# Optimization experiments

Hardware: AMD Instinct MI355X
Metric: run time of the kernel (lower is better)

## Reference

```python
import jax, jax.numpy as jnp
import numpy as np

TAU_MEM = 20.0
V_THRESH = 1.0
DECAY = float(np.exp(-1.0 / TAU_MEM))
SLOPE = 5.0  # fast-sigmoid surrogate slope


@jax.custom_vjp
def spike(x):
    # Heaviside spike with fast-sigmoid surrogate gradient
    return (x > 0).astype(x.dtype)

def _spike_fwd(x):
    return spike(x), x

def _spike_bwd(x, g):
    surr = 1.0 / (1.0 + SLOPE * jnp.abs(x)) ** 2
    return (g * surr,)

spike.defvjp(_spike_fwd, _spike_bwd)


def setup_inputs() -> dict:
    key = jax.random.key(0)
    k1, k2 = jax.random.split(key)
    B, T, n_in, n_out = 32, 1000, 1024, 512
    input_spikes_seq = (jax.random.uniform(k1, (B, T, n_in)) < 0.05).astype(jnp.float32)
    w_init_scale = 0.5
    W = jax.random.normal(k2, (n_out, n_in), dtype=jnp.float32) * (w_init_scale / np.sqrt(n_in))
    return {"input_spikes_seq": input_spikes_seq, "W": W}


def reference(input_spikes_seq, W):
    # input_spikes_seq: (B, T, n_in); W: (n_out, n_in) -> out: (B, T, n_out)
    B, T, _ = input_spikes_seq.shape
    n_out = W.shape[0]
    # Hoist the GEMM out of the time loop: (B,T,n_in) x (n_out,n_in) -> (B,T,n_out)
    I = jnp.einsum('bti,oi->bto', input_spikes_seq, W)
    I_t = jnp.transpose(I, (1, 0, 2))  # (T, B, n_out)

    def step(v, i_t):
        v = v * DECAY + i_t
        s = spike(v - V_THRESH)
        v = v * (1.0 - jax.lax.stop_gradient(s))  # reset, detached as in torch
        return v, s

    v0 = jnp.zeros((B, n_out), dtype=input_spikes_seq.dtype)
    _, out_t = jax.lax.scan(step, v0, I_t)  # out_t: (T, B, n_out)
    return jnp.transpose(out_t, (1, 0, 2))
```

## Files before the change

### kernel.cpp

```cpp
#include <hip/hip_runtime.h>


#define N_IN   1024
#define N_OUT  512
#define DECAY_F 0.95122942450071400910f
#define SCALE     17179869184.0
#define SCALE_INV 5.8207660913467407e-11f

typedef int  v4i  __attribute__((ext_vector_type(4)));
typedef int  v16i __attribute__((ext_vector_type(16)));

__global__ __launch_bounds__(256) void s_to_i8(const float* __restrict__ S,
                                               signed char* __restrict__ S8,
                                               int n16) {
    const int g = blockIdx.x * 256 + threadIdx.x;
    if (g >= n16) return;
    const float4* p = reinterpret_cast<const float4*>(S) + (size_t)g * 4;
    union { signed char c[16]; int4 v; } u;
#pragma unroll
    for (int q = 0; q < 4; ++q) {
        const float4 v = p[q];
        u.c[q * 4 + 0] = (signed char)(v.x != 0.f);
        u.c[q * 4 + 1] = (signed char)(v.y != 0.f);
        u.c[q * 4 + 2] = (signed char)(v.z != 0.f);
        u.c[q * 4 + 3] = (signed char)(v.w != 0.f);
    }
    reinterpret_cast<int4*>(S8)[g] = u.v;
}

__global__ __launch_bounds__(256) void w_digits(const float* __restrict__ W,
                                                signed char* __restrict__ D8) {
    const int n  = blockIdx.x;
    const int k0 = threadIdx.x * 4;
    const float4 wv = *reinterpret_cast<const float4*>(W + (size_t)n * N_IN + k0);
    const float ww[4] = {wv.x, wv.y, wv.z, wv.w};
    int pk[4] = {0, 0, 0, 0};
#pragma unroll
    for (int j = 0; j < 4; ++j) {
        long long wi = (long long)rint((double)ww[j] * SCALE);
        const int d0 = (int)((wi + 128) & 255) - 128; wi = (wi - d0) >> 8;
        const int d1 = (int)((wi + 128) & 255) - 128; wi = (wi - d1) >> 8;
        const int d2 = (int)((wi + 128) & 255) - 128; wi = (wi - d2) >> 8;
        const int d3 = (int)wi;
        pk[0] |= (d0 & 255) << (8 * j);
        pk[1] |= (d1 & 255) << (8 * j);
        pk[2] |= (d2 & 255) << (8 * j);
        pk[3] |= (d3 & 255) << (8 * j);
    }
#pragma unroll
    for (int d = 0; d < 4; ++d)
        *reinterpret_cast<int*>(D8 + (size_t)(d * N_OUT + n) * N_IN + k0) = pk[d];
}

#define BM 256
#define BN 64
#define BK 64
#define PITCH 80
#define ABUF (BM * PITCH)
#define ASH(buf) (lds + (buf) * ABUF)
#define BSH(buf) (lds + 2 * ABUF + (buf) * ABUF)

__global__ __launch_bounds__(512, 2) void gemm_i8(
        const signed char* __restrict__ S8,
        const signed char* __restrict__ D8,
        float* __restrict__ I, int M) {
    extern __shared__ signed char lds[];

    const int tid  = threadIdx.x;
    const int lane = tid & 63;
    const int w    = tid >> 6;
    const int wwm  = w >> 1;
    const int wwn  = w & 1;

    const int nx  = M / BM;
    const int u   = (blockIdx.x & 7) * nx + (blockIdx.x >> 3);
    const int bm  = u >> 3;
    const int bn  = u & 7;
    const int m0 = bm * BM;
    const int n0 = bn * BN;

    const int srow = tid >> 2;
    const int scol = (tid & 3) * 16;

    v16i acc[2][4];
#pragma unroll
    for (int mf = 0; mf < 2; ++mf)
#pragma unroll
        for (int d = 0; d < 4; ++d)
#pragma unroll
            for (int i = 0; i < 16; ++i) acc[mf][d][i] = 0;

    int4 pa0, pa1, pb0, pb1;
    int4 qa0, qa1, qb0, qb1;

#define LOADT(SET, kt)                                                            \
    SET##a0 = *reinterpret_cast<const int4*>(S8 + (size_t)(m0 + srow) * N_IN + (kt) * BK + scol);        \
    SET##a1 = *reinterpret_cast<const int4*>(S8 + (size_t)(m0 + srow + 128) * N_IN + (kt) * BK + scol);  \
    SET##b0 = *reinterpret_cast<const int4*>(D8 + (size_t)(((srow >> 6) * N_OUT) + n0 + (srow & 63)) * N_IN + (kt) * BK + scol);            \
    SET##b1 = *reinterpret_cast<const int4*>(D8 + (size_t)(((srow >> 6) * N_OUT + 2 * N_OUT) + n0 + (srow & 63)) * N_IN + (kt) * BK + scol);

#define WRITET(buf, SET)                                                          \
    *reinterpret_cast<int4*>(ASH(buf) + (srow) * PITCH + scol) = SET##a0;         \
    *reinterpret_cast<int4*>(ASH(buf) + (srow + 128) * PITCH + scol) = SET##a1;   \
    *reinterpret_cast<int4*>(BSH(buf) + (srow) * PITCH + scol) = SET##b0;         \
    *reinterpret_cast<int4*>(BSH(buf) + (srow + 128) * PITCH + scol) = SET##b1;

    const int fr = lane & 31;
    const int kh = (lane >> 5) * 16;

#define COMPUTE(buf)                                                              \
    _Pragma("unroll")                                                             \
    for (int ksub = 0; ksub < 2; ++ksub) {                                        \
        const int kb = ksub * 32 + kh;                                            \
        v4i af0 = *reinterpret_cast<const v4i*>(ASH(buf) + (wwm * 64 + fr) * PITCH + kb);       \
        v4i af1 = *reinterpret_cast<const v4i*>(ASH(buf) + (wwm * 64 + 32 + fr) * PITCH + kb);  \
        v4i bf[4];                                                                \
        _Pragma("unroll")                                                         \
        for (int d = 0; d < 4; ++d)                                               \
            bf[d] = *reinterpret_cast<const v4i*>(BSH(buf) + (d * 64 + wwn * 32 + fr) * PITCH + kb); \
        __builtin_amdgcn_s_setprio(1);                                            \
        _Pragma("unroll")                                                         \
        for (int d = 0; d < 4; ++d) {                                             \
            acc[0][d] = __builtin_amdgcn_mfma_i32_32x32x32_i8(af0, bf[d], acc[0][d], 0, 0, 0); \
            acc[1][d] = __builtin_amdgcn_mfma_i32_32x32x32_i8(af1, bf[d], acc[1][d], 0, 0, 0); \
        }                                                                         \
        __builtin_amdgcn_s_setprio(0);                                            \
    }

    LOADT(p, 0);
    WRITET(0, p);
    LOADT(p, 1);
    LOADT(q, 2);
    __syncthreads();

#pragma unroll 1
    for (int kt = 0; kt < 16; kt += 2) {
        WRITET(1, p);
        if (kt + 3 <= 15) { LOADT(p, kt + 3); }
        COMPUTE(0);
        __syncthreads();
        if (kt + 2 <= 15) {
            WRITET(0, q);
            if (kt + 4 <= 15) { LOADT(q, kt + 4); }
        }
        COMPUTE(1);
        __syncthreads();
    }

    const int col = fr;
    const int rb_ = (lane >> 5) * 4;
#pragma unroll
    for (int mf = 0; mf < 2; ++mf) {
#pragma unroll
        for (int reg = 0; reg < 16; ++reg) {
            const int row = (reg & 3) + 8 * (reg >> 2) + rb_;
            const long long v =
                ((long long)acc[mf][3][reg] << 24) + ((long long)acc[mf][2][reg] << 16) +
                ((long long)acc[mf][1][reg] << 8) + (long long)acc[mf][0][reg];
            I[(size_t)(m0 + wwm * 64 + mf * 32 + row) * N_OUT + n0 + wwn * 32 + col] =
                (float)v * SCALE_INV;
        }
    }
}
#undef LOADT
#undef WRITET
#undef COMPUTE

#define UT 50
__global__ __launch_bounds__(64) void lif_scan3(float* __restrict__ IO, int T) {
    const int idx = blockIdx.x * 64 + threadIdx.x;
    const int b = idx >> 9, o = idx & (N_OUT - 1);
    float* p = IO + (size_t)b * T * N_OUT + o;
    float ca[UT], cb[UT];
    float v = 0.f;
#pragma unroll
    for (int j = 0; j < UT; ++j) ca[j] = p[(size_t)j * N_OUT];
#pragma unroll 1
    for (int t0 = 0; t0 < T; t0 += 2 * UT) {
        if (t0 + UT < T) {
#pragma unroll
            for (int j = 0; j < UT; ++j) cb[j] = p[(size_t)(t0 + UT + j) * N_OUT];
        }
#pragma unroll
        for (int j = 0; j < UT; ++j) {
            v = v * DECAY_F + ca[j];
            float s = (v > 1.0f) ? 1.0f : 0.f;
            v *= (1.f - s);
            ca[j] = s;
        }
#pragma unroll
        for (int j = 0; j < UT; ++j) p[(size_t)(t0 + j) * N_OUT] = ca[j];
        if (t0 + UT >= T) break;
        if (t0 + 2 * UT < T) {
#pragma unroll
            for (int j = 0; j < UT; ++j) ca[j] = p[(size_t)(t0 + 2 * UT + j) * N_OUT];
        }
#pragma unroll
        for (int j = 0; j < UT; ++j) {
            v = v * DECAY_F + cb[j];
            float s = (v > 1.0f) ? 1.0f : 0.f;
            v *= (1.f - s);
            cb[j] = s;
        }
#pragma unroll
        for (int j = 0; j < UT; ++j) p[(size_t)(t0 + UT + j) * N_OUT] = cb[j];
    }
}

__global__ __launch_bounds__(256) void transpose_w(const float* __restrict__ W,
                                                   float* __restrict__ WT) {
    __shared__ float t[32][33];
    const int k0 = blockIdx.x * 32;
    const int n0 = blockIdx.y * 32;
    const int lx = threadIdx.x & 31;
    const int ly = threadIdx.x >> 5;
#pragma unroll
    for (int r = ly; r < 32; r += 8)
        t[r][lx] = W[(size_t)(n0 + r) * N_IN + k0 + lx];
    __syncthreads();
#pragma unroll
    for (int r = ly; r < 32; r += 8)
        WT[(size_t)(k0 + r) * N_OUT + n0 + lx] = t[lx][r];
}

__global__ __launch_bounds__(256) void gather_rows(
        const float* __restrict__ S, const float* __restrict__ WT,
        float* __restrict__ I, int M) {
    const int wid  = blockIdx.x * 4 + (threadIdx.x >> 6);
    const int lane = threadIdx.x & 63;
    if (wid >= M) return;
    const float* srow = S + (size_t)wid * N_IN;
    float4 a0 = {0.f, 0.f, 0.f, 0.f};
    float4 a1 = {0.f, 0.f, 0.f, 0.f};
    float sv[16];
#pragma unroll
    for (int g = 0; g < 16; ++g) sv[g] = srow[g * 64 + lane];
#pragma unroll
    for (int g = 0; g < 16; ++g) {
        unsigned long long m = __ballot(sv[g] != 0.0f);
        while (m) {
            const int b = __builtin_ctzll(m);
            m &= m - 1;
            const int k = g * 64 + b;
            const float* wp = WT + (size_t)k * N_OUT + lane * 4;
            const float4 w0 = *reinterpret_cast<const float4*>(wp);
            const float4 w1 = *reinterpret_cast<const float4*>(wp + 256);
            a0.x += w0.x; a0.y += w0.y; a0.z += w0.z; a0.w += w0.w;
            a1.x += w1.x; a1.y += w1.y; a1.z += w1.z; a1.w += w1.w;
        }
    }
    float* op = I + (size_t)wid * N_OUT + lane * 4;
    *reinterpret_cast<float4*>(op) = a0;
    *reinterpret_cast<float4*>(op + 256) = a1;
}

extern "C" void kernel_launch(void* const* d_in, const int* in_sizes, int n_in,
                              void* d_out, int out_size, void* d_ws, size_t ws_size,
                              hipStream_t stream) {
    const float* S = (const float*)d_in[0];
    const float* W = (const float*)d_in[1];
    float* out = (float*)d_out;

    const int K = N_IN;
    const int M = in_sizes[0] / K;
    const int B = 32;
    const int T = M / B;

    const size_t s8_bytes = (size_t)M * N_IN;
    const size_t d8_bytes = (size_t)4 * N_OUT * N_IN;
    const size_t need = s8_bytes + d8_bytes;

    if (ws_size >= need && (M % BM) == 0) {
        signed char* S8 = (signed char*)d_ws;
        signed char* D8 = (signed char*)d_ws + s8_bytes;
        const int n16 = M * N_IN / 16;
        s_to_i8<<<(n16 + 255) / 256, 256, 0, stream>>>(S, S8, n16);
        w_digits<<<N_OUT, 256, 0, stream>>>(W, D8);
        const size_t lds_bytes = (size_t)4 * ABUF;
        gemm_i8<<<(M / BM) * (N_OUT / BN), 512, lds_bytes, stream>>>(S8, D8, out, M);
        lif_scan3<<<(B * N_OUT) / 64, 64, 0, stream>>>(out, T);
    } else if (ws_size >= (size_t)N_IN * N_OUT * sizeof(float) && (M % 4) == 0) {
        float* WT = (float*)d_ws;
        dim3 tg(N_IN / 32, N_OUT / 32);
        transpose_w<<<tg, 256, 0, stream>>>(W, WT);
        gather_rows<<<M / 4, 256, 0, stream>>>(S, WT, out, M);
        lif_scan3<<<(B * N_OUT) / 64, 64, 0, stream>>>(out, T);
    }
}
```

Before: 147.5 us.

## Shrink GEMM block to 128 rows with 256 threads and deepen scan unroll

Halves the GEMM M-tile from 256 to 128 rows and drops the block to 256 threads. It replaces the two-set register prefetch (p/q, three tiles ahead) with a single set one tile ahead, packs A and B into one buffer per stage, and fixes the grid swizzle for the larger block count. The LIF scan's register chunk grows from 50 to 100 timesteps with launch bounds of one block. This trades load depth and A-tile reuse for more blocks, and the bigger scan chunk may raise register pressure or spill.

```diff
diff --git a/kernel.cpp b/kernel.cpp
--- a/kernel.cpp
+++ b/kernel.cpp
@@ -52,15 +52,17 @@
         *reinterpret_cast<int*>(D8 + (size_t)(d * N_OUT + n) * N_IN + k0) = pk[d];
 }
 
-#define BM 256
+#define BM 128
 #define BN 64
 #define BK 64
 #define PITCH 80
-#define ABUF (BM * PITCH)
-#define ASH(buf) (lds + (buf) * ABUF)
-#define BSH(buf) (lds + 2 * ABUF + (buf) * ABUF)
-
-__global__ __launch_bounds__(512, 2) void gemm_i8(
+#define A_ROWS 128
+#define B_ROWS 256
+#define BUFSZ ((A_ROWS + B_ROWS) * PITCH)
+#define ASH(buf) (lds + (buf) * BUFSZ)
+#define BSH(buf) (lds + (buf) * BUFSZ + A_ROWS * PITCH)
+
+__global__ __launch_bounds__(256, 2) void gemm_i8(
         const signed char* __restrict__ S8,
         const signed char* __restrict__ D8,
         float* __restrict__ I, int M) {
@@ -72,7 +74,7 @@
     const int wwm  = w >> 1;
     const int wwn  = w & 1;
 
-    const int nx  = M / BM;
+    const int nx  = (M / BM) * (N_OUT / BN) / 8;
     const int u   = (blockIdx.x & 7) * nx + (blockIdx.x >> 3);
     const int bm  = u >> 3;
     const int bn  = u & 7;
@@ -90,20 +92,23 @@
 #pragma unroll
             for (int i = 0; i < 16; ++i) acc[mf][d][i] = 0;
 
-    int4 pa0, pa1, pb0, pb1;
-    int4 qa0, qa1, qb0, qb1;
-
-#define LOADT(SET, kt)                                                            \
-    SET##a0 = *reinterpret_cast<const int4*>(S8 + (size_t)(m0 + srow) * N_IN + (kt) * BK + scol);        \
-    SET##a1 = *reinterpret_cast<const int4*>(S8 + (size_t)(m0 + srow + 128) * N_IN + (kt) * BK + scol);  \
-    SET##b0 = *reinterpret_cast<const int4*>(D8 + (size_t)(((srow >> 6) * N_OUT) + n0 + (srow & 63)) * N_IN + (kt) * BK + scol);            \
-    SET##b1 = *reinterpret_cast<const int4*>(D8 + (size_t)(((srow >> 6) * N_OUT + 2 * N_OUT) + n0 + (srow & 63)) * N_IN + (kt) * BK + scol);
-
-#define WRITET(buf, SET)                                                          \
-    *reinterpret_cast<int4*>(ASH(buf) + (srow) * PITCH + scol) = SET##a0;         \
-    *reinterpret_cast<int4*>(ASH(buf) + (srow + 128) * PITCH + scol) = SET##a1;   \
-    *reinterpret_cast<int4*>(BSH(buf) + (srow) * PITCH + scol) = SET##b0;         \
-    *reinterpret_cast<int4*>(BSH(buf) + (srow + 128) * PITCH + scol) = SET##b1;
+    int4 pa0, pa1, pb0, pb1, pb2, pb3;
+
+#define LOADT(kt)                                                                 \
+    pa0 = *reinterpret_cast<const int4*>(S8 + (size_t)(m0 + srow) * N_IN + (kt) * BK + scol);       \
+    pa1 = *reinterpret_cast<const int4*>(S8 + (size_t)(m0 + srow + 64) * N_IN + (kt) * BK + scol);  \
+    pb0 = *reinterpret_cast<const int4*>(D8 + (size_t)(0 * N_OUT + n0 + srow) * N_IN + (kt) * BK + scol); \
+    pb1 = *reinterpret_cast<const int4*>(D8 + (size_t)(1 * N_OUT + n0 + srow) * N_IN + (kt) * BK + scol); \
+    pb2 = *reinterpret_cast<const int4*>(D8 + (size_t)(2 * N_OUT + n0 + srow) * N_IN + (kt) * BK + scol); \
+    pb3 = *reinterpret_cast<const int4*>(D8 + (size_t)(3 * N_OUT + n0 + srow) * N_IN + (kt) * BK + scol);
+
+#define WRITET(buf)                                                               \
+    *reinterpret_cast<int4*>(ASH(buf) + (srow) * PITCH + scol) = pa0;             \
+    *reinterpret_cast<int4*>(ASH(buf) + (srow + 64) * PITCH + scol) = pa1;        \
+    *reinterpret_cast<int4*>(BSH(buf) + (srow) * PITCH + scol) = pb0;             \
+    *reinterpret_cast<int4*>(BSH(buf) + (srow + 64) * PITCH + scol) = pb1;        \
+    *reinterpret_cast<int4*>(BSH(buf) + (srow + 128) * PITCH + scol) = pb2;       \
+    *reinterpret_cast<int4*>(BSH(buf) + (srow + 192) * PITCH + scol) = pb3;
 
     const int fr = lane & 31;
     const int kh = (lane >> 5) * 16;
@@ -127,21 +132,20 @@
         __builtin_amdgcn_s_setprio(0);                                            \
     }
 
-    LOADT(p, 0);
-    WRITET(0, p);
-    LOADT(p, 1);
-    LOADT(q, 2);
+    LOADT(0);
+    WRITET(0);
+    LOADT(1);
     __syncthreads();
 
 #pragma unroll 1
     for (int kt = 0; kt < 16; kt += 2) {
-        WRITET(1, p);
-        if (kt + 3 <= 15) { LOADT(p, kt + 3); }
+        WRITET(1);
+        if (kt + 2 <= 15) { LOADT(kt + 2); }
         COMPUTE(0);
         __syncthreads();
         if (kt + 2 <= 15) {
-            WRITET(0, q);
-            if (kt + 4 <= 15) { LOADT(q, kt + 4); }
+            WRITET(0);
+            if (kt + 3 <= 15) { LOADT(kt + 3); }
         }
         COMPUTE(1);
         __syncthreads();
@@ -166,8 +170,8 @@
 #undef WRITET
 #undef COMPUTE
 
-#define UT 50
-__global__ __launch_bounds__(64) void lif_scan3(float* __restrict__ IO, int T) {
+#define UT 100
+__global__ __launch_bounds__(64, 1) void lif_scan3(float* __restrict__ IO, int T) {
     const int idx = blockIdx.x * 64 + threadIdx.x;
     const int b = idx >> 9, o = idx & (N_OUT - 1);
     float* p = IO + (size_t)b * T * N_OUT + o;
@@ -270,14 +274,14 @@
     const size_t d8_bytes = (size_t)4 * N_OUT * N_IN;
     const size_t need = s8_bytes + d8_bytes;
 
-    if (ws_size >= need && (M % BM) == 0) {
+    if (ws_size >= need && (M % BM) == 0 && ((M / BM) * (N_OUT / BN)) % 8 == 0) {
         signed char* S8 = (signed char*)d_ws;
         signed char* D8 = (signed char*)d_ws + s8_bytes;
         const int n16 = M * N_IN / 16;
         s_to_i8<<<(n16 + 255) / 256, 256, 0, stream>>>(S, S8, n16);
         w_digits<<<N_OUT, 256, 0, stream>>>(W, D8);
-        const size_t lds_bytes = (size_t)4 * ABUF;
-        gemm_i8<<<(M / BM) * (N_OUT / BN), 512, lds_bytes, stream>>>(S8, D8, out, M);
+        const size_t lds_bytes = (size_t)2 * BUFSZ;
+        gemm_i8<<<(M / BM) * (N_OUT / BN), 256, lds_bytes, stream>>>(S8, D8, out, M);
         lif_scan3<<<(B * N_OUT) / 64, 64, 0, stream>>>(out, T);
     } else if (ws_size >= (size_t)N_IN * N_OUT * sizeof(float) && (M % 4) == 0) {
         float* WT = (float*)d_ws;
```

Measured after the change: 147.3 us. No clear change (-0.1%).

## Fuse int8 GEMM with LIF scan, keeping per-batch currents in LDS

Applied to the files above, without the earlier changes.

Replaces the separate GEMM and LIF scan kernels with one fused kernel. Each block owns one batch and a 64-column output slice. It loops over time chunks of 256, stages the int32-to-float currents in LDS, runs the membrane recurrence there and writes only the spikes to global memory. This removes the global write and re-read of the full current tensor and one launch. In exchange, each block walks time chunks serially, only 64 threads per block do the scan while the rest wait at barriers, and occupancy drops to one block per CU. The grid is also fixed at 256 blocks.

```diff
diff --git a/kernel.cpp b/kernel.cpp
--- a/kernel.cpp
+++ b/kernel.cpp
@@ -59,12 +59,14 @@
 #define ABUF (BM * PITCH)
 #define ASH(buf) (lds + (buf) * ABUF)
 #define BSH(buf) (lds + 2 * ABUF + (buf) * ABUF)
-
-__global__ __launch_bounds__(512, 2) void gemm_i8(
+#define IPITCH 260
+
+__global__ __launch_bounds__(512, 1) void fused_gemm_scan(
         const signed char* __restrict__ S8,
         const signed char* __restrict__ D8,
-        float* __restrict__ I, int M) {
+        float* __restrict__ out, int T) {
     extern __shared__ signed char lds[];
+    float* LDSI = (float*)(lds + 4 * ABUF);
 
     const int tid  = threadIdx.x;
     const int lane = tid & 63;
@@ -72,23 +74,19 @@
     const int wwm  = w >> 1;
     const int wwn  = w & 1;
 
-    const int nx  = M / BM;
-    const int u   = (blockIdx.x & 7) * nx + (blockIdx.x >> 3);
-    const int bm  = u >> 3;
-    const int bn  = u & 7;
-    const int m0 = bm * BM;
-    const int n0 = bn * BN;
+    const int xcd = blockIdx.x & 7;
+    const int loc = blockIdx.x >> 3;
+    const int b   = xcd * 4 + (loc >> 3);
+    const int n0  = (loc & 7) * BN;
 
     const int srow = tid >> 2;
     const int scol = (tid & 3) * 16;
-
-    v16i acc[2][4];
-#pragma unroll
-    for (int mf = 0; mf < 2; ++mf)
-#pragma unroll
-        for (int d = 0; d < 4; ++d)
-#pragma unroll
-            for (int i = 0; i < 16; ++i) acc[mf][d][i] = 0;
+    const int fr = lane & 31;
+    const int kh = (lane >> 5) * 16;
+
+    const int NC = (T + BM - 1) / BM;
+    const int so = w * 8 + (lane & 7);
+    float vmem = 0.f;
 
     int4 pa0, pa1, pb0, pb1;
     int4 qa0, qa1, qb0, qb1;
@@ -104,9 +102,6 @@
     *reinterpret_cast<int4*>(ASH(buf) + (srow + 128) * PITCH + scol) = SET##a1;   \
     *reinterpret_cast<int4*>(BSH(buf) + (srow) * PITCH + scol) = SET##b0;         \
     *reinterpret_cast<int4*>(BSH(buf) + (srow + 128) * PITCH + scol) = SET##b1;
-
-    const int fr = lane & 31;
-    const int kh = (lane >> 5) * 16;
 
 #define COMPUTE(buf)                                                              \
     _Pragma("unroll")                                                             \
@@ -127,85 +122,93 @@
         __builtin_amdgcn_s_setprio(0);                                            \
     }
 
-    LOADT(p, 0);
-    WRITET(0, p);
-    LOADT(p, 1);
-    LOADT(q, 2);
-    __syncthreads();
-
 #pragma unroll 1
-    for (int kt = 0; kt < 16; kt += 2) {
-        WRITET(1, p);
-        if (kt + 3 <= 15) { LOADT(p, kt + 3); }
-        COMPUTE(0);
+    for (int tc = 0; tc < NC; ++tc) {
+        const int m0 = b * T + tc * BM;
+        const int CL = min(BM, T - tc * BM);
+
+        v16i acc[2][4];
+#pragma unroll
+        for (int mf = 0; mf < 2; ++mf)
+#pragma unroll
+            for (int d = 0; d < 4; ++d)
+#pragma unroll
+                for (int i = 0; i < 16; ++i) acc[mf][d][i] = 0;
+
+        LOADT(p, 0);
+        WRITET(0, p);
+        LOADT(p, 1);
+        LOADT(q, 2);
         __syncthreads();
-        if (kt + 2 <= 15) {
-            WRITET(0, q);
-            if (kt + 4 <= 15) { LOADT(q, kt + 4); }
-        }
-        COMPUTE(1);
+
+#pragma unroll 1
+        for (int kt = 0; kt < 16; kt += 2) {
+            WRITET(1, p);
+            if (kt + 3 <= 15) { LOADT(p, kt + 3); }
+            COMPUTE(0);
+            __syncthreads();
+            if (kt + 2 <= 15) {
+                WRITET(0, q);
+                if (kt + 4 <= 15) { LOADT(q, kt + 4); }
+            }
+            COMPUTE(1);
+            __syncthreads();
+        }
+
+        const int colo = wwn * 32 + fr;
+        const int rb_ = (lane >> 5) * 4;
+#pragma unroll
+        for (int mf = 0; mf < 2; ++mf) {
+#pragma unroll
+            for (int q = 0; q < 4; ++q) {
+                float tv[4];
+#pragma unroll
+                for (int j = 0; j < 4; ++j) {
+                    const int reg = q * 4 + j;
+                    const long long v =
+                        ((long long)acc[mf][3][reg] << 24) + ((long long)acc[mf][2][reg] << 16) +
+                        ((long long)acc[mf][1][reg] << 8) + (long long)acc[mf][0][reg];
+                    tv[j] = (float)v * SCALE_INV;
+                }
+                const int t0 = wwm * 64 + mf * 32 + q * 8 + rb_;
+                float4 f4; f4.x = tv[0]; f4.y = tv[1]; f4.z = tv[2]; f4.w = tv[3];
+                *reinterpret_cast<float4*>(&LDSI[colo * IPITCH + t0]) = f4;
+            }
+        }
         __syncthreads();
-    }
-
-    const int col = fr;
-    const int rb_ = (lane >> 5) * 4;
-#pragma unroll
-    for (int mf = 0; mf < 2; ++mf) {
-#pragma unroll
-        for (int reg = 0; reg < 16; ++reg) {
-            const int row = (reg & 3) + 8 * (reg >> 2) + rb_;
-            const long long v =
-                ((long long)acc[mf][3][reg] << 24) + ((long long)acc[mf][2][reg] << 16) +
-                ((long long)acc[mf][1][reg] << 8) + (long long)acc[mf][0][reg];
-            I[(size_t)(m0 + wwm * 64 + mf * 32 + row) * N_OUT + n0 + wwn * 32 + col] =
-                (float)v * SCALE_INV;
+
+        if ((lane & 63) < 8) {
+            float vv = vmem;
+#pragma unroll 1
+            for (int t0 = 0; t0 < CL; t0 += 8) {
+                float c[8];
+#pragma unroll
+                for (int j = 0; j < 8; ++j)
+                    c[j] = (t0 + j < CL) ? LDSI[so * IPITCH + t0 + j] : 0.f;
+#pragma unroll
+                for (int j = 0; j < 8; ++j) {
+                    vv = vv * DECAY_F + c[j];
+                    float s = (vv > 1.0f) ? 1.0f : 0.f;
+                    vv *= (1.f - s);
+                    c[j] = s;
+                }
+#pragma unroll
+                for (int j = 0; j < 8; ++j)
+                    if (t0 + j < CL) LDSI[so * IPITCH + t0 + j] = c[j];
+            }
+            vmem = vv;
+        }
+        __syncthreads();
+
+        for (int i = tid; i < CL * BN; i += 512) {
+            const int row = i >> 6, col = i & 63;
+            out[(size_t)(m0 + row) * N_OUT + n0 + col] = LDSI[col * IPITCH + row];
         }
     }
 }
 #undef LOADT
 #undef WRITET
 #undef COMPUTE
-
-#define UT 50
-__global__ __launch_bounds__(64) void lif_scan3(float* __restrict__ IO, int T) {
-    const int idx = blockIdx.x * 64 + threadIdx.x;
-    const int b = idx >> 9, o = idx & (N_OUT - 1);
-    float* p = IO + (size_t)b * T * N_OUT + o;
-    float ca[UT], cb[UT];
-    float v = 0.f;
-#pragma unroll
-    for (int j = 0; j < UT; ++j) ca[j] = p[(size_t)j * N_OUT];
-#pragma unroll 1
-    for (int t0 = 0; t0 < T; t0 += 2 * UT) {
-        if (t0 + UT < T) {
-#pragma unroll
-            for (int j = 0; j < UT; ++j) cb[j] = p[(size_t)(t0 + UT + j) * N_OUT];
-        }
-#pragma unroll
-        for (int j = 0; j < UT; ++j) {
-            v = v * DECAY_F + ca[j];
-            float s = (v > 1.0f) ? 1.0f : 0.f;
-            v *= (1.f - s);
-            ca[j] = s;
-        }
-#pragma unroll
-        for (int j = 0; j < UT; ++j) p[(size_t)(t0 + j) * N_OUT] = ca[j];
-        if (t0 + UT >= T) break;
-        if (t0 + 2 * UT < T) {
-#pragma unroll
-            for (int j = 0; j < UT; ++j) ca[j] = p[(size_t)(t0 + 2 * UT + j) * N_OUT];
-        }
-#pragma unroll
-        for (int j = 0; j < UT; ++j) {
-            v = v * DECAY_F + cb[j];
-            float s = (v > 1.0f) ? 1.0f : 0.f;
-            v *= (1.f - s);
-            cb[j] = s;
-        }
-#pragma unroll
-        for (int j = 0; j < UT; ++j) p[(size_t)(t0 + UT + j) * N_OUT] = cb[j];
-    }
-}
 
 __global__ __launch_bounds__(256) void transpose_w(const float* __restrict__ W,
                                                    float* __restrict__ WT) {
@@ -239,9 +242,9 @@
     for (int g = 0; g < 16; ++g) {
         unsigned long long m = __ballot(sv[g] != 0.0f);
         while (m) {
-            const int b = __builtin_ctzll(m);
+            const int bb = __builtin_ctzll(m);
             m &= m - 1;
-            const int k = g * 64 + b;
+            const int k = g * 64 + bb;
             const float* wp = WT + (size_t)k * N_OUT + lane * 4;
             const float4 w0 = *reinterpret_cast<const float4*>(wp);
             const float4 w1 = *reinterpret_cast<const float4*>(wp + 256);
@@ -252,6 +255,47 @@
     float* op = I + (size_t)wid * N_OUT + lane * 4;
     *reinterpret_cast<float4*>(op) = a0;
     *reinterpret_cast<float4*>(op + 256) = a1;
+}
+
+#define UT 50
+__global__ __launch_bounds__(64) void lif_scan3(float* __restrict__ IO, int T) {
+    const int idx = blockIdx.x * 64 + threadIdx.x;
+    const int b = idx >> 9, o = idx & (N_OUT - 1);
+    float* p = IO + (size_t)b * T * N_OUT + o;
+    float ca[UT], cb[UT];
+    float v = 0.f;
+#pragma unroll
+    for (int j = 0; j < UT; ++j) ca[j] = p[(size_t)j * N_OUT];
+#pragma unroll 1
+    for (int t0 = 0; t0 < T; t0 += 2 * UT) {
+        if (t0 + UT < T) {
+#pragma unroll
+            for (int j = 0; j < UT; ++j) cb[j] = p[(size_t)(t0 + UT + j) * N_OUT];
+        }
+#pragma unroll
+        for (int j = 0; j < UT; ++j) {
+            v = v * DECAY_F + ca[j];
+            float s = (v > 1.0f) ? 1.0f : 0.f;
+            v *= (1.f - s);
+            ca[j] = s;
+        }
+#pragma unroll
+        for (int j = 0; j < UT; ++j) p[(size_t)(t0 + j) * N_OUT] = ca[j];
+        if (t0 + UT >= T) break;
+        if (t0 + 2 * UT < T) {
+#pragma unroll
+            for (int j = 0; j < UT; ++j) ca[j] = p[(size_t)(t0 + 2 * UT + j) * N_OUT];
+        }
+#pragma unroll
+        for (int j = 0; j < UT; ++j) {
+            v = v * DECAY_F + cb[j];
+            float s = (v > 1.0f) ? 1.0f : 0.f;
+            v *= (1.f - s);
+            cb[j] = s;
+        }
+#pragma unroll
+        for (int j = 0; j < UT; ++j) p[(size_t)(t0 + UT + j) * N_OUT] = cb[j];
+    }
 }
 
 extern "C" void kernel_launch(void* const* d_in, const int* in_sizes, int n_in,
@@ -270,15 +314,14 @@
     const size_t d8_bytes = (size_t)4 * N_OUT * N_IN;
     const size_t need = s8_bytes + d8_bytes;
 
-    if (ws_size >= need && (M % BM) == 0) {
+    if (ws_size >= need && (M % B) == 0) {
         signed char* S8 = (signed char*)d_ws;
         signed char* D8 = (signed char*)d_ws + s8_bytes;
         const int n16 = M * N_IN / 16;
         s_to_i8<<<(n16 + 255) / 256, 256, 0, stream>>>(S, S8, n16);
         w_digits<<<N_OUT, 256, 0, stream>>>(W, D8);
-        const size_t lds_bytes = (size_t)4 * ABUF;
-        gemm_i8<<<(M / BM) * (N_OUT / BN), 512, lds_bytes, stream>>>(S8, D8, out, M);
-        lif_scan3<<<(B * N_OUT) / 64, 64, 0, stream>>>(out, T);
+        const size_t lds_bytes = (size_t)4 * ABUF + 64 * IPITCH * 4;
+        fused_gemm_scan<<<256, 512, lds_bytes, stream>>>(S8, D8, out, T);
     } else if (ws_size >= (size_t)N_IN * N_OUT * sizeof(float) && (M % 4) == 0) {
         float* WT = (float*)d_ws;
         dim3 tg(N_IN / 32, N_OUT / 32);
```

After: 155.7 us. +5.6%, slower.

## Stage GEMM tiles via direct global-to-LDS loads with triple buffering and swizzle

Applied to the files above, without the earlier changes.

The int8 GEMM now loads its tiles with global_load_lds straight into LDS, replacing the register round-trip. It uses a three-buffer ring with vmcnt waits and one barrier per k-step instead of double buffering with two barriers. An XOR swizzle replaces the padded pitch to avoid bank conflicts. The two prep kernels are also merged into one launch to save a kernel launch. Together these risk occupancy changes from the 96KB LDS footprint and depend on the hand-written vmcnt accounting being correct.

```diff
diff --git a/kernel.cpp b/kernel.cpp
--- a/kernel.cpp
+++ b/kernel.cpp
@@ -10,55 +10,59 @@
 typedef int  v4i  __attribute__((ext_vector_type(4)));
 typedef int  v16i __attribute__((ext_vector_type(16)));
 
-__global__ __launch_bounds__(256) void s_to_i8(const float* __restrict__ S,
-                                               signed char* __restrict__ S8,
-                                               int n16) {
-    const int g = blockIdx.x * 256 + threadIdx.x;
-    if (g >= n16) return;
-    const float4* p = reinterpret_cast<const float4*>(S) + (size_t)g * 4;
-    union { signed char c[16]; int4 v; } u;
-#pragma unroll
-    for (int q = 0; q < 4; ++q) {
-        const float4 v = p[q];
-        u.c[q * 4 + 0] = (signed char)(v.x != 0.f);
-        u.c[q * 4 + 1] = (signed char)(v.y != 0.f);
-        u.c[q * 4 + 2] = (signed char)(v.z != 0.f);
-        u.c[q * 4 + 3] = (signed char)(v.w != 0.f);
-    }
-    reinterpret_cast<int4*>(S8)[g] = u.v;
-}
-
-__global__ __launch_bounds__(256) void w_digits(const float* __restrict__ W,
-                                                signed char* __restrict__ D8) {
-    const int n  = blockIdx.x;
-    const int k0 = threadIdx.x * 4;
-    const float4 wv = *reinterpret_cast<const float4*>(W + (size_t)n * N_IN + k0);
-    const float ww[4] = {wv.x, wv.y, wv.z, wv.w};
-    int pk[4] = {0, 0, 0, 0};
-#pragma unroll
-    for (int j = 0; j < 4; ++j) {
-        long long wi = (long long)rint((double)ww[j] * SCALE);
-        const int d0 = (int)((wi + 128) & 255) - 128; wi = (wi - d0) >> 8;
-        const int d1 = (int)((wi + 128) & 255) - 128; wi = (wi - d1) >> 8;
-        const int d2 = (int)((wi + 128) & 255) - 128; wi = (wi - d2) >> 8;
-        const int d3 = (int)wi;
-        pk[0] |= (d0 & 255) << (8 * j);
-        pk[1] |= (d1 & 255) << (8 * j);
-        pk[2] |= (d2 & 255) << (8 * j);
-        pk[3] |= (d3 & 255) << (8 * j);
-    }
-#pragma unroll
-    for (int d = 0; d < 4; ++d)
-        *reinterpret_cast<int*>(D8 + (size_t)(d * N_OUT + n) * N_IN + k0) = pk[d];
+typedef __attribute__((address_space(1))) const void gv_t;
+typedef __attribute__((address_space(3))) void lv_t;
+__device__ __forceinline__ void gl16(const signed char* g, signed char* l) {
+    __builtin_amdgcn_global_load_lds((gv_t*)g, (lv_t*)l, 16, 0, 0);
+}
+
+__global__ __launch_bounds__(256) void prep(const float* __restrict__ S,
+                                            signed char* __restrict__ S8,
+                                            const float* __restrict__ W,
+                                            signed char* __restrict__ D8,
+                                            int nS16blocks) {
+    if ((int)blockIdx.x < nS16blocks) {
+        const int g = blockIdx.x * 256 + threadIdx.x;
+        const float4* p = reinterpret_cast<const float4*>(S) + (size_t)g * 4;
+        union { signed char c[16]; int4 v; } u;
+#pragma unroll
+        for (int q = 0; q < 4; ++q) {
+            const float4 v = p[q];
+            u.c[q * 4 + 0] = (signed char)(v.x != 0.f);
+            u.c[q * 4 + 1] = (signed char)(v.y != 0.f);
+            u.c[q * 4 + 2] = (signed char)(v.z != 0.f);
+            u.c[q * 4 + 3] = (signed char)(v.w != 0.f);
+        }
+        reinterpret_cast<int4*>(S8)[g] = u.v;
+    } else {
+        const int n  = blockIdx.x - nS16blocks;
+        const int k0 = threadIdx.x * 4;
+        const float4 wv = *reinterpret_cast<const float4*>(W + (size_t)n * N_IN + k0);
+        const float ww[4] = {wv.x, wv.y, wv.z, wv.w};
+        int pk[4] = {0, 0, 0, 0};
+#pragma unroll
+        for (int j = 0; j < 4; ++j) {
+            long long wi = (long long)rint((double)ww[j] * SCALE);
+            const int d0 = (int)((wi + 128) & 255) - 128; wi = (wi - d0) >> 8;
+            const int d1 = (int)((wi + 128) & 255) - 128; wi = (wi - d1) >> 8;
+            const int d2 = (int)((wi + 128) & 255) - 128; wi = (wi - d2) >> 8;
+            const int d3 = (int)wi;
+            pk[0] |= (d0 & 255) << (8 * j);
+            pk[1] |= (d1 & 255) << (8 * j);
+            pk[2] |= (d2 & 255) << (8 * j);
+            pk[3] |= (d3 & 255) << (8 * j);
+        }
+#pragma unroll
+        for (int d = 0; d < 4; ++d)
+            *reinterpret_cast<int*>(D8 + (size_t)(d * N_OUT + n) * N_IN + k0) = pk[d];
+    }
 }
 
 #define BM 256
 #define BN 64
 #define BK 64
-#define PITCH 80
-#define ABUF (BM * PITCH)
-#define ASH(buf) (lds + (buf) * ABUF)
-#define BSH(buf) (lds + 2 * ABUF + (buf) * ABUF)
+#define TILEB (BM * BK)
+#define BUFSZ (2 * TILEB)
 
 __global__ __launch_bounds__(512, 2) void gemm_i8(
         const signed char* __restrict__ S8,
@@ -79,8 +83,27 @@
     const int m0 = bm * BM;
     const int n0 = bn * BN;
 
-    const int srow = tid >> 2;
-    const int scol = (tid & 3) * 16;
+    const int lrow  = lane >> 2;
+    const int sslot = (lane & 3) << 4;
+    const int swzs  = ((lrow >> 1) & 3) << 4;
+    const int scola = sslot ^ swzs;
+
+    const signed char* aSrc0 = S8 + (size_t)(m0 + w * 16 + lrow) * N_IN + scola;
+    const signed char* aSrc1 = aSrc0 + (size_t)128 * N_IN;
+    const signed char* bSrc0 = D8 + (size_t)((w >> 2) * N_OUT + n0 + (w & 3) * 16 + lrow) * N_IN + scola;
+    const signed char* bSrc1 = bSrc0 + (size_t)2 * N_OUT * N_IN;
+
+    const int aDst0 = (w * 16) * 64;
+    const int aDst1 = aDst0 + 128 * 64;
+    const int bDst0 = TILEB + (w * 16) * 64;
+    const int bDst1 = bDst0 + 128 * 64;
+
+#define STAGE(bofs, kt) do {                                      \
+        gl16(aSrc0 + (kt) * BK, lds + (bofs) + aDst0);            \
+        gl16(aSrc1 + (kt) * BK, lds + (bofs) + aDst1);            \
+        gl16(bSrc0 + (kt) * BK, lds + (bofs) + bDst0);            \
+        gl16(bSrc1 + (kt) * BK, lds + (bofs) + bDst1);            \
+    } while (0)
 
     v16i acc[2][4];
 #pragma unroll
@@ -89,35 +112,21 @@
         for (int d = 0; d < 4; ++d)
 #pragma unroll
             for (int i = 0; i < 16; ++i) acc[mf][d][i] = 0;
-
-    int4 pa0, pa1, pb0, pb1;
-    int4 qa0, qa1, qb0, qb1;
-
-#define LOADT(SET, kt)                                                            \
-    SET##a0 = *reinterpret_cast<const int4*>(S8 + (size_t)(m0 + srow) * N_IN + (kt) * BK + scol);        \
-    SET##a1 = *reinterpret_cast<const int4*>(S8 + (size_t)(m0 + srow + 128) * N_IN + (kt) * BK + scol);  \
-    SET##b0 = *reinterpret_cast<const int4*>(D8 + (size_t)(((srow >> 6) * N_OUT) + n0 + (srow & 63)) * N_IN + (kt) * BK + scol);            \
-    SET##b1 = *reinterpret_cast<const int4*>(D8 + (size_t)(((srow >> 6) * N_OUT + 2 * N_OUT) + n0 + (srow & 63)) * N_IN + (kt) * BK + scol);
-
-#define WRITET(buf, SET)                                                          \
-    *reinterpret_cast<int4*>(ASH(buf) + (srow) * PITCH + scol) = SET##a0;         \
-    *reinterpret_cast<int4*>(ASH(buf) + (srow + 128) * PITCH + scol) = SET##a1;   \
-    *reinterpret_cast<int4*>(BSH(buf) + (srow) * PITCH + scol) = SET##b0;         \
-    *reinterpret_cast<int4*>(BSH(buf) + (srow + 128) * PITCH + scol) = SET##b1;
 
     const int fr = lane & 31;
     const int kh = (lane >> 5) * 16;
-
-#define COMPUTE(buf)                                                              \
+    const int swzr = ((fr >> 1) & 3) << 4;
+
+#define COMPUTE(bofs)                                                             \
     _Pragma("unroll")                                                             \
     for (int ksub = 0; ksub < 2; ++ksub) {                                        \
-        const int kb = ksub * 32 + kh;                                            \
-        v4i af0 = *reinterpret_cast<const v4i*>(ASH(buf) + (wwm * 64 + fr) * PITCH + kb);       \
-        v4i af1 = *reinterpret_cast<const v4i*>(ASH(buf) + (wwm * 64 + 32 + fr) * PITCH + kb);  \
+        const int kbx = (ksub * 32 + kh) ^ swzr;                                  \
+        v4i af0 = *reinterpret_cast<const v4i*>(lds + (bofs) + (wwm * 64 + fr) * 64 + kbx);      \
+        v4i af1 = *reinterpret_cast<const v4i*>(lds + (bofs) + (wwm * 64 + 32 + fr) * 64 + kbx); \
         v4i bf[4];                                                                \
         _Pragma("unroll")                                                         \
         for (int d = 0; d < 4; ++d)                                               \
-            bf[d] = *reinterpret_cast<const v4i*>(BSH(buf) + (d * 64 + wwn * 32 + fr) * PITCH + kb); \
+            bf[d] = *reinterpret_cast<const v4i*>(lds + (bofs) + TILEB + (d * 64 + wwn * 32 + fr) * 64 + kbx); \
         __builtin_amdgcn_s_setprio(1);                                            \
         _Pragma("unroll")                                                         \
         for (int d = 0; d < 4; ++d) {                                             \
@@ -127,24 +136,18 @@
         __builtin_amdgcn_s_setprio(0);                                            \
     }
 
-    LOADT(p, 0);
-    WRITET(0, p);
-    LOADT(p, 1);
-    LOADT(q, 2);
-    __syncthreads();
+    STAGE(0, 0);
+    STAGE(BUFSZ, 1);
+    int bo0 = 0, bo1 = BUFSZ, bo2 = 2 * BUFSZ;
 
 #pragma unroll 1
-    for (int kt = 0; kt < 16; kt += 2) {
-        WRITET(1, p);
-        if (kt + 3 <= 15) { LOADT(p, kt + 3); }
-        COMPUTE(0);
+    for (int kt = 0; kt < 16; ++kt) {
+        if (kt < 15) asm volatile("s_waitcnt vmcnt(4)" ::: "memory");
+        else         asm volatile("s_waitcnt vmcnt(0)" ::: "memory");
         __syncthreads();
-        if (kt + 2 <= 15) {
-            WRITET(0, q);
-            if (kt + 4 <= 15) { LOADT(q, kt + 4); }
-        }
-        COMPUTE(1);
-        __syncthreads();
+        if (kt + 2 <= 15) { STAGE(bo2, kt + 2); }
+        COMPUTE(bo0);
+        const int t = bo0; bo0 = bo1; bo1 = bo2; bo2 = t;
     }
 
     const int col = fr;
@@ -162,8 +165,7 @@
         }
     }
 }
-#undef LOADT
-#undef WRITET
+#undef STAGE
 #undef COMPUTE
 
 #define UT 50
@@ -239,9 +241,9 @@
     for (int g = 0; g < 16; ++g) {
         unsigned long long m = __ballot(sv[g] != 0.0f);
         while (m) {
-            const int b = __builtin_ctzll(m);
+            const int bb = __builtin_ctzll(m);
             m &= m - 1;
-            const int k = g * 64 + b;
+            const int k = g * 64 + bb;
             const float* wp = WT + (size_t)k * N_OUT + lane * 4;
             const float4 w0 = *reinterpret_cast<const float4*>(wp);
             const float4 w1 = *reinterpret_cast<const float4*>(wp + 256);
@@ -270,13 +272,12 @@
     const size_t d8_bytes = (size_t)4 * N_OUT * N_IN;
     const size_t need = s8_bytes + d8_bytes;
 
-    if (ws_size >= need && (M % BM) == 0) {
+    if (ws_size >= need && (M % BM) == 0 && ((M / BM) * (N_OUT / BN)) % 8 == 0) {
         signed char* S8 = (signed char*)d_ws;
         signed char* D8 = (signed char*)d_ws + s8_bytes;
-        const int n16 = M * N_IN / 16;
-        s_to_i8<<<(n16 + 255) / 256, 256, 0, stream>>>(S, S8, n16);
-        w_digits<<<N_OUT, 256, 0, stream>>>(W, D8);
-        const size_t lds_bytes = (size_t)4 * ABUF;
+        const int nS16blocks = (M * N_IN / 16) / 256;
+        prep<<<nS16blocks + N_OUT, 256, 0, stream>>>(S, S8, W, D8, nS16blocks);
+        const size_t lds_bytes = (size_t)3 * BUFSZ;
         gemm_i8<<<(M / BM) * (N_OUT / BN), 512, lds_bytes, stream>>>(S8, D8, out, M);
         lif_scan3<<<(B * N_OUT) / 64, 64, 0, stream>>>(out, T);
     } else if (ws_size >= (size_t)N_IN * N_OUT * sizeof(float) && (M % 4) == 0) {
```

Measured after the change: 146.8 us. No clear change (-0.4%).
